# Performance work log

Hardware: AMD Instinct MI355X
Metric: run time of the kernel (lower is better)

## Reference

```python
import jax, jax.numpy as jnp
import numpy as np
import math

B, T, D, H = 4, 1024, 1024, 16
DK = D // H
TAU_THRESH = 0.3


def setup_inputs() -> dict:
    key = jax.random.key(0)
    ks = jax.random.split(key, 13)
    s = 1.0 / math.sqrt(D)
    return {
        "x": jax.random.normal(ks[0], (B, T, D), dtype=jnp.float32),
        "Wq": jax.random.normal(ks[1], (D, D), dtype=jnp.float32) * s,
        "bq": jax.random.normal(ks[2], (D,), dtype=jnp.float32) * s,
        "Wk": jax.random.normal(ks[3], (D, D), dtype=jnp.float32) * s,
        "bk": jax.random.normal(ks[4], (D,), dtype=jnp.float32) * s,
        "Wv": jax.random.normal(ks[5], (D, D), dtype=jnp.float32) * s,
        "bv": jax.random.normal(ks[6], (D,), dtype=jnp.float32) * s,
        "Wo": jax.random.normal(ks[7], (D, D), dtype=jnp.float32) * s,
        "bo": jax.random.normal(ks[8], (D,), dtype=jnp.float32) * s,
        "Wg1": jax.random.normal(ks[9], (1, D), dtype=jnp.float32) * s,
        "bg1": jax.random.normal(ks[10], (1,), dtype=jnp.float32) * s,
        "Wg2": jax.random.normal(ks[11], (1, D), dtype=jnp.float32) * s,
        "bg2": jax.random.normal(ks[12], (1,), dtype=jnp.float32) * s,
    }


def reference(x, Wq, bq, Wk, bk, Wv, bv, Wo, bo, Wg1, bg1, Wg2, bg2):
    b, t, d = x.shape
    # projections (torch Linear: y = x @ W.T + b)
    Q = (x @ Wq.T + bq).reshape(b, t, H, DK).transpose(0, 2, 1, 3)  # [B,H,T,dk]
    K = (x @ Wk.T + bk).reshape(b, t, H, DK).transpose(0, 2, 1, 3)
    V = (x @ Wv.T + bv).reshape(b, t, H, DK).transpose(0, 2, 1, 3)
    scores = jnp.einsum("bhqd,bhkd->bhqk", Q, K) / math.sqrt(DK)  # [B,H,T,T]
    # confidence gates from first-token query context [B, H*dk] = [B, D]
    context = Q[:, :, 0, :].reshape(b, d)
    q1 = jax.nn.sigmoid(context @ Wg1.T + bg1)  # [B,1]
    q2 = jax.nn.sigmoid(context @ Wg2.T + bg2)  # [B,1]
    c = jnp.clip(q1 * q2, 1e-8, 1.0)            # [B,1]
    tau = jnp.where(c < TAU_THRESH, 1.0 / c, jnp.ones_like(c)).reshape(b, 1, 1, 1)
    p = jax.nn.softmax(scores / tau, axis=-1)
    cb = c.reshape(b, 1, 1, 1)
    p_gated = cb * p + (1.0 - cb) * (1.0 / t)
    u = jnp.mean(1.0 - c, axis=-1, keepdims=True)  # [B,1]
    attn_out = jnp.einsum("bhqk,bhkd->bhqd", p_gated, V)
    attn_out = attn_out.transpose(0, 2, 1, 3).reshape(b, t, d)
    output = attn_out @ Wo.T + bo
    return output, u
```

## Files before the change

kernel.cpp:

```cpp
#include <hip/hip_runtime.h>
#include <stdint.h>

typedef short bf16x8 __attribute__((ext_vector_type(8)));
typedef float f32x4 __attribute__((ext_vector_type(4)));

#define MFMA_BF16(a, b, c) __builtin_amdgcn_mfma_f32_16x16x32_bf16((a), (b), (c), 0, 0, 0)

__device__ __forceinline__ short f2bf(float x) {
  union { float f; uint32_t u; } v; v.f = x;
  uint32_t r = (v.u + 0x7FFFu + ((v.u >> 16) & 1u)) >> 16;
  return (short)r;
}
__device__ __forceinline__ uint32_t rnd_bf_hi(float x) {
  union { float f; uint32_t u; } v; v.f = x;
  return v.u + 0x7FFFu + ((v.u >> 16) & 1u);
}
__device__ __forceinline__ uint32_t pack2bf(float a, float b) {
  return __builtin_amdgcn_perm(rnd_bf_hi(b), rnd_bf_hi(a), 0x07060302);
}
__device__ __forceinline__ float bfbits2f(uint32_t b16) {
  union { uint32_t u; float f; } v; v.u = b16 << 16; return v.f;
}
__device__ __forceinline__ float fexp2(float x) {
#if __has_builtin(__builtin_amdgcn_exp2f)
  return __builtin_amdgcn_exp2f(x);
#else
  return __expf(x * 0.6931471805599453f);
#endif
}
__device__ __forceinline__ void async16(const void* g, void* l) {
  __builtin_amdgcn_global_load_lds(
      (const __attribute__((address_space(1))) uint32_t*)g,
      (__attribute__((address_space(3))) uint32_t*)l, 16, 0, 0);
}

__global__ __launch_bounds__(256) void prep_k(
    const float* __restrict__ x, const float* __restrict__ Wq,
    const float* __restrict__ Wk, const float* __restrict__ Wv,
    const float* __restrict__ Wo, const float* __restrict__ bq,
    short* __restrict__ xb, short* __restrict__ Wqb, short* __restrict__ Wkb,
    short* __restrict__ Wvb, short* __restrict__ Wob, float* __restrict__ ctx) {
  __shared__ float xs[1024];
  const int bid = blockIdx.x;
  const int tid = threadIdx.x;
  if (bid < 8192) {
    const float* src; short* dst; int idx;
    if (bid < 4096) {
      src = x; dst = xb; idx = (bid << 8) + tid;
    } else {
      const int r = bid - 4096;
      const int z = r >> 10;
      src = (z == 0) ? Wq : (z == 1) ? Wk : (z == 2) ? Wv : Wo;
      dst = (z == 0) ? Wqb : (z == 1) ? Wkb : (z == 2) ? Wvb : Wob;
      idx = ((r & 1023) << 8) + tid;
    }
    float4 v = ((const float4*)src)[idx];
    short4 o;
    o.x = f2bf(v.x); o.y = f2bf(v.y); o.z = f2bf(v.z); o.w = f2bf(v.w);
    ((short4*)dst)[idx] = o;
  } else {
    const int r = bid - 8192;
    const int b = r >> 4;
    const int n0 = (r & 15) << 6;
    for (int i = tid; i < 1024; i += 256) xs[i] = x[b * 1048576 + i];
    __syncthreads();
    const int w = tid >> 6, lane = tid & 63;
    const float4* xv4 = (const float4*)xs;
    for (int rr = 0; rr < 16; ++rr) {
      const int n = n0 + (w << 4) + rr;
      const float4* wrow = (const float4*)(Wq + n * 1024);
      float p = 0.f;
#pragma unroll
      for (int c2 = 0; c2 < 4; ++c2) {
        float4 wv = wrow[lane + (c2 << 6)];
        float4 xv = xv4[lane + (c2 << 6)];
        p += xv.x * wv.x + xv.y * wv.y + xv.z * wv.z + xv.w * wv.w;
      }
#pragma unroll
      for (int off = 32; off; off >>= 1) p += __shfl_xor(p, off);
      if (lane == 0) ctx[b * 1024 + n] = p + bq[n];
    }
  }
}

__global__ __launch_bounds__(256) void gates_fin(const float* __restrict__ ctx,
                                                 const float* __restrict__ Wg1,
                                                 const float* __restrict__ bg1,
                                                 const float* __restrict__ Wg2,
                                                 const float* __restrict__ bg2,
                                                 float* __restrict__ gates,
                                                 float* __restrict__ u_out) {
  __shared__ float red[16];
  const int tid = threadIdx.x, w = tid >> 6, lane = tid & 63;
  for (int b = 0; b < 4; ++b) {
    float4 cv = ((const float4*)(ctx + b * 1024))[tid];
    float4 w1 = ((const float4*)Wg1)[tid];
    float4 w2 = ((const float4*)Wg2)[tid];
    float p1 = cv.x * w1.x + cv.y * w1.y + cv.z * w1.z + cv.w * w1.w;
    float p2 = cv.x * w2.x + cv.y * w2.y + cv.z * w2.z + cv.w * w2.w;
#pragma unroll
    for (int off = 32; off; off >>= 1) { p1 += __shfl_xor(p1, off); p2 += __shfl_xor(p2, off); }
    if (lane == 0) { red[w] = p1; red[8 + w] = p2; }
    __syncthreads();
    if (tid == 0) {
      float g1 = red[0] + red[1] + red[2] + red[3] + bg1[0];
      float g2 = red[8] + red[9] + red[10] + red[11] + bg2[0];
      float q1 = 1.f / (1.f + expf(-g1));
      float q2 = 1.f / (1.f + expf(-g2));
      float c = fminf(fmaxf(q1 * q2, 1e-8f), 1.0f);
      gates[b * 2 + 0] = c;
      gates[b * 2 + 1] = (c < 0.3f ? c : 1.0f) * 0.125f;
      u_out[b] = 1.0f - c;
    }
    __syncthreads();
  }
}

__global__ __launch_bounds__(256) void gemm_qkv(
    const short* __restrict__ xb,
    const short* __restrict__ Wqb, const short* __restrict__ Wkb, const short* __restrict__ Wvb,
    const float* __restrict__ bq, const float* __restrict__ bk, const float* __restrict__ bv,
    const float* __restrict__ gat,
    short* __restrict__ Qh, short* __restrict__ Kh, short* __restrict__ Vt) {
  const int z = blockIdx.z;
  const short* W = (z == 0) ? Wqb : (z == 1) ? Wkb : Wvb;
  const float* bias = (z == 0) ? bq : (z == 1) ? bk : bv;

  const int m0 = blockIdx.x << 7;
  const int n0 = blockIdx.y << 7;
  const int tid = threadIdx.x;
  const int w = tid >> 6, lane = tid & 63;
  const int m15 = lane & 15, quad = lane >> 4;
  const int wr = w >> 1, wc = w & 1;

  const float qsc = (z == 0) ? gat[(m0 >> 10) * 2 + 1] * 1.4426950408889634f : 1.0f;

  __shared__ short As[4096];
  __shared__ short Bs[4096];

  f32x4 acc[4][4];
#pragma unroll
  for (int i = 0; i < 4; ++i)
#pragma unroll
    for (int j = 0; j < 4; ++j) { f32x4 zz = {0.f, 0.f, 0.f, 0.f}; acc[i][j] = zz; }

  const int s0 = tid, s1 = tid + 256;
  const int row0 = s0 >> 2, lcb0 = (s0 & 3) ^ ((row0 >> 1) & 3);
  const int row1 = s1 >> 2, lcb1 = (s1 & 3) ^ ((row1 >> 1) & 3);
  const short* ga0 = xb + (m0 + row0) * 1024 + (lcb0 << 3);
  const short* ga1 = xb + (m0 + row1) * 1024 + (lcb1 << 3);
  const short* gb0 = W + (n0 + row0) * 1024 + (lcb0 << 3);
  const short* gb1 = W + (n0 + row1) * 1024 + (lcb1 << 3);
  short* la0 = &As[s0 << 3];
  short* la1 = &As[s1 << 3];
  short* lb0 = &Bs[s0 << 3];
  short* lb1 = &Bs[s1 << 3];

  for (int kt = 0; kt < 32; ++kt) {
    async16(ga0, la0); async16(ga1, la1);
    async16(gb0, lb0); async16(gb1, lb1);
    ga0 += 32; ga1 += 32; gb0 += 32; gb1 += 32;
    __syncthreads();
    bf16x8 a[4], b[4];
#pragma unroll
    for (int i = 0; i < 4; ++i) {
      const int ra = (wr << 6) + (i << 4) + m15;
      a[i] = *(const bf16x8*)(&As[ra * 32 + ((quad ^ ((ra >> 1) & 3)) << 3)]);
    }
#pragma unroll
    for (int j = 0; j < 4; ++j) {
      const int rb = (wc << 6) + (j << 4) + m15;
      b[j] = *(const bf16x8*)(&Bs[rb * 32 + ((quad ^ ((rb >> 1) & 3)) << 3)]);
    }
#pragma unroll
    for (int i = 0; i < 4; ++i)
#pragma unroll
      for (int j = 0; j < 4; ++j)
        acc[i][j] = MFMA_BF16(a[i], b[j], acc[i][j]);
    __syncthreads();
  }

  if (z == 2) {
    const int batch = m0 >> 10;
#pragma unroll
    for (int j = 0; j < 4; ++j) {
      const int n = n0 + (wc << 6) + (j << 4) + m15;
      const float bb_ = bias[n];
      const int h = n >> 6, dk = n & 63;
      short* vrow = Vt + ((((batch << 4) + h) << 6) + dk) * 1024;
#pragma unroll
      for (int i = 0; i < 4; ++i) {
        const int t = (m0 & 1023) + (wr << 6) + (i << 4) + (quad << 2);
        uint2 pk;
        pk.x = pack2bf(acc[i][j][0] + bb_, acc[i][j][1] + bb_);
        pk.y = pack2bf(acc[i][j][2] + bb_, acc[i][j][3] + bb_);
        *(uint2*)(vrow + t) = pk;
      }
    }
  } else {
#pragma unroll
    for (int j = 0; j < 4; ++j) {
      const int n = n0 + (wc << 6) + (j << 4) + m15;
      const float bb_ = bias[n];
      const int h = n >> 6, dk = n & 63;
#pragma unroll
      for (int i = 0; i < 4; ++i) {
        const int mb = m0 + (wr << 6) + (i << 4) + (quad << 2);
#pragma unroll
        for (int r = 0; r < 4; ++r) {
          const int m = mb + r;
          const int batch = m >> 10, t = m & 1023;
          const short o = f2bf((acc[i][j][r] + bb_) * qsc);
          if (z == 1) Kh[((batch * 16 + h) * 1024 + t) * 64 + dk] = o;
          else        Qh[((batch * 16 + h) * 1024 + t) * 64 + dk] = o;
        }
      }
    }
  }
}

__global__ __launch_bounds__(256) void gemm_out(const short* __restrict__ Ab,
                                                const short* __restrict__ Wo,
                                                const float* __restrict__ bo,
                                                float* __restrict__ Cout) {
  const int m0 = blockIdx.x << 6;
  const int n0 = blockIdx.y << 7;
  const int tid = threadIdx.x;
  const int w = tid >> 6, lane = tid & 63;
  const int m15 = lane & 15, quad = lane >> 4;
  const int wr = w >> 1, wc = w & 1;

  __shared__ short As[2048];
  __shared__ short Bs[4096];

  f32x4 acc[2][4];
#pragma unroll
  for (int i = 0; i < 2; ++i)
#pragma unroll
    for (int j = 0; j < 4; ++j) { f32x4 zz = {0.f, 0.f, 0.f, 0.f}; acc[i][j] = zz; }

  const int s0 = tid, s1 = tid + 256;
  const int arow = s0 >> 2, alcb = (s0 & 3) ^ ((arow >> 1) & 3);
  const int brow0 = s0 >> 2, blcb0 = alcb;
  const int brow1 = s1 >> 2, blcb1 = (s1 & 3) ^ ((brow1 >> 1) & 3);
  const short* gA  = Ab + (m0 + arow) * 1024 + (alcb << 3);
  const short* gB0 = Wo + (n0 + brow0) * 1024 + (blcb0 << 3);
  const short* gB1 = Wo + (n0 + brow1) * 1024 + (blcb1 << 3);
  short* lA  = &As[s0 << 3];
  short* lB0 = &Bs[s0 << 3];
  short* lB1 = &Bs[s1 << 3];

  for (int kt = 0; kt < 32; ++kt) {
    async16(gA, lA);
    async16(gB0, lB0); async16(gB1, lB1);
    gA += 32; gB0 += 32; gB1 += 32;
    __syncthreads();
    bf16x8 a[2], b[4];
#pragma unroll
    for (int i = 0; i < 2; ++i) {
      const int ra = (wr << 5) + (i << 4) + m15;
      a[i] = *(const bf16x8*)(&As[ra * 32 + ((quad ^ ((ra >> 1) & 3)) << 3)]);
    }
#pragma unroll
    for (int j = 0; j < 4; ++j) {
      const int rb = (wc << 6) + (j << 4) + m15;
      b[j] = *(const bf16x8*)(&Bs[rb * 32 + ((quad ^ ((rb >> 1) & 3)) << 3)]);
    }
#pragma unroll
    for (int i = 0; i < 2; ++i)
#pragma unroll
      for (int j = 0; j < 4; ++j)
        acc[i][j] = MFMA_BF16(a[i], b[j], acc[i][j]);
    __syncthreads();
  }

#pragma unroll
  for (int j = 0; j < 4; ++j) {
    const int n = n0 + (wc << 6) + (j << 4) + m15;
    const float bb_ = bo[n];
#pragma unroll
    for (int i = 0; i < 2; ++i) {
      const int mb = m0 + (wr << 5) + (i << 4) + (quad << 2);
#pragma unroll
      for (int r = 0; r < 4; ++r)
        Cout[(mb + r) * 1024 + n] = acc[i][j][r] + bb_;
    }
  }
}

__global__ __launch_bounds__(256) void meanv_k(const short* __restrict__ Vt,
                                               float* __restrict__ meanV) {
  const int bh = blockIdx.x;
  const int tid = threadIdx.x;
  const int d = tid >> 2, part = tid & 3;
  const short* row = Vt + bh * 65536 + d * 1024 + part * 256;
  float s = 0.f;
#pragma unroll 4
  for (int i = 0; i < 64; ++i) {
    uint2 v = *(const uint2*)(row + i * 4);
    s += bfbits2f(v.x & 0xffffu) + bfbits2f(v.x >> 16) +
         bfbits2f(v.y & 0xffffu) + bfbits2f(v.y >> 16);
  }
  s += __shfl_xor(s, 1);
  s += __shfl_xor(s, 2);
  if (part == 0) meanV[bh * 64 + d] = s * (1.0f / 1024.0f);
}

__global__ __launch_bounds__(256, 4) void attn_k(const short* __restrict__ Qh,
                                                 const short* __restrict__ Kh,
                                                 const short* __restrict__ Vt,
                                                 const float* __restrict__ gates,
                                                 const float* __restrict__ meanV,
                                                 short* __restrict__ attnb) {
  const int bh = blockIdx.x;
  const int b = bh >> 4, h = bh & 15;
  const int q0 = blockIdx.y << 6;
  const int tid = threadIdx.x;
  const int w = tid >> 6, lane = tid & 63;
  const int m15 = lane & 15, quad = lane >> 4;

  __shared__ short Ks[2][4096];
  __shared__ short Vs[2][4096];

  const short* ksrc = Kh + bh * 65536;
  const short* vsrc = Vt + bh * 65536;

  const short* qsrc = Qh + ((bh << 10) + q0 + (w << 4) + m15) * 64;
  const bf16x8 qb0 = *(const bf16x8*)(qsrc + (quad << 3));
  const bf16x8 qb1 = *(const bf16x8*)(qsrc + 32 + (quad << 3));

  const int off0 = tid, off1 = tid + 256;
  const int r0 = off0 >> 3, cb0 = (off0 & 7) ^ (r0 & 7);
  const int r1 = off1 >> 3, cb1 = (off1 & 7) ^ (r1 & 7);

#define STAGE(kv, bufi)                                                        \
  do {                                                                         \
    async16(ksrc + (((kv) << 6) + r0) * 64 + (cb0 << 3), &Ks[bufi][off0 << 3]);\
    async16(ksrc + (((kv) << 6) + r1) * 64 + (cb1 << 3), &Ks[bufi][off1 << 3]);\
    async16(vsrc + r0 * 1024 + ((kv) << 6) + (cb0 << 3), &Vs[bufi][off0 << 3]);\
    async16(vsrc + r1 * 1024 + ((kv) << 6) + (cb1 << 3), &Vs[bufi][off1 << 3]);\
  } while (0)

  STAGE(0, 0);

  float lsum = 0.f;
  f32x4 o_acc[4];
#pragma unroll
  for (int jd = 0; jd < 4; ++jd) { f32x4 zz = {0.f, 0.f, 0.f, 0.f}; o_acc[jd] = zz; }

  const int srcA = ((quad & 1) << 5) + m15;
  const int srcB = srcA + 16;
  const bool selhi = (quad & 2) != 0;

  for (int kv = 0; kv < 16; ++kv) {
    __syncthreads();
    if (kv < 15) STAGE(kv + 1, (kv + 1) & 1);
    const short* Kb = &Ks[kv & 1][0];
    const short* Vb = &Vs[kv & 1][0];

    f32x4 sacc[4];
#pragma unroll
    for (int s = 0; s < 4; ++s) {
      const int row = (s << 4) + m15;
      const int sw = row & 7;
      bf16x8 a0 = *(const bf16x8*)(Kb + (row << 6) + ((quad ^ sw) << 3));
      bf16x8 a1 = *(const bf16x8*)(Kb + (row << 6) + (((quad + 4) ^ sw) << 3));
      f32x4 zz = {0.f, 0.f, 0.f, 0.f};
      zz = MFMA_BF16(a0, qb0, zz);
      zz = MFMA_BF16(a1, qb1, zz);
      sacc[s] = zz;
    }

    uint32_t pk[4][2];
#pragma unroll
    for (int s = 0; s < 4; ++s) {
      float p0 = fexp2(sacc[s][0]);
      float p1 = fexp2(sacc[s][1]);
      float p2 = fexp2(sacc[s][2]);
      float p3 = fexp2(sacc[s][3]);
      lsum += (p0 + p1) + (p2 + p3);
      pk[s][0] = pack2bf(p0, p1);
      pk[s][1] = pack2bf(p2, p3);
    }

    bf16x8 pf[2];
#pragma unroll
    for (int H = 0; H < 2; ++H) {
      uint32_t f[4];
#pragma unroll
      for (int rp = 0; rp < 2; ++rp) {
        uint32_t alo = (uint32_t)__shfl((int)pk[2 * H][rp], srcA);
        uint32_t ahi = (uint32_t)__shfl((int)pk[2 * H + 1][rp], srcA);
        uint32_t blo = (uint32_t)__shfl((int)pk[2 * H][rp], srcB);
        uint32_t bhi = (uint32_t)__shfl((int)pk[2 * H + 1][rp], srcB);
        f[rp]     = selhi ? ahi : alo;
        f[2 + rp] = selhi ? bhi : blo;
      }
      pf[H] = *(bf16x8*)f;
    }

#pragma unroll
    for (int jd = 0; jd < 4; ++jd) {
      const int row = (jd << 4) + m15;
      const int sw = row & 7;
      bf16x8 v0 = *(const bf16x8*)(Vb + (row << 6) + ((quad ^ sw) << 3));
      bf16x8 v1 = *(const bf16x8*)(Vb + (row << 6) + (((quad + 4) ^ sw) << 3));
      o_acc[jd] = MFMA_BF16(v0, pf[0], o_acc[jd]);
      o_acc[jd] = MFMA_BF16(v1, pf[1], o_acc[jd]);
    }
  }
#undef STAGE

  float l = lsum;
  l += __shfl_xor(l, 16);
  l += __shfl_xor(l, 32);

  const float cg = gates[b * 2 + 0];
  const float s0 = cg / l;
  const float omc = 1.0f - cg;
  const int qrow = q0 + (w << 4) + m15;
  short* orow = attnb + ((b << 10) + qrow) * 1024 + (h << 6);
#pragma unroll
  for (int jd = 0; jd < 4; ++jd) {
    float4 mv = *(const float4*)(meanV + (bh << 6) + (jd << 4) + (quad << 2));
    float v0_ = s0 * o_acc[jd][0] + omc * mv.x;
    float v1_ = s0 * o_acc[jd][1] + omc * mv.y;
    float v2_ = s0 * o_acc[jd][2] + omc * mv.z;
    float v3_ = s0 * o_acc[jd][3] + omc * mv.w;
    uint2 st;
    st.x = pack2bf(v0_, v1_);
    st.y = pack2bf(v2_, v3_);
    *(uint2*)(orow + (jd << 4) + (quad << 2)) = st;
  }
}

extern "C" void kernel_launch(void* const* d_in, const int* in_sizes, int n_in,
                              void* d_out, int out_size, void* d_ws, size_t ws_size,
                              hipStream_t stream) {
  const float* x   = (const float*)d_in[0];
  const float* Wq  = (const float*)d_in[1];
  const float* bq  = (const float*)d_in[2];
  const float* Wk  = (const float*)d_in[3];
  const float* bk  = (const float*)d_in[4];
  const float* Wv  = (const float*)d_in[5];
  const float* bv  = (const float*)d_in[6];
  const float* Wo  = (const float*)d_in[7];
  const float* bo  = (const float*)d_in[8];
  const float* Wg1 = (const float*)d_in[9];
  const float* bg1 = (const float*)d_in[10];
  const float* Wg2 = (const float*)d_in[11];
  const float* bg2 = (const float*)d_in[12];
  float* out = (float*)d_out;

  char* ws = (char*)d_ws;
  short* xb   = (short*)(ws + 0);
  short* Wqb  = (short*)(ws + 8388608);
  short* Wkb  = (short*)(ws + 10485760);
  short* Wvb  = (short*)(ws + 12582912);
  short* Wob  = (short*)(ws + 14680064);
  short* Qh   = (short*)(ws + 16777216);
  short* Kh   = (short*)(ws + 25165824);
  short* Vt   = (short*)(ws + 33554432);
  short* attb = (short*)(ws + 41943040);
  float* ctx  = (float*)(ws + 50331648);
  float* gat  = (float*)(ws + 50348032);
  float* mV   = (float*)(ws + 50348064);

  prep_k<<<8256, 256, 0, stream>>>(x, Wq, Wk, Wv, Wo, bq,
                                   xb, Wqb, Wkb, Wvb, Wob, ctx);
  gates_fin<<<1, 256, 0, stream>>>(ctx, Wg1, bg1, Wg2, bg2, gat, out + 4194304);

  gemm_qkv<<<dim3(32, 8, 3), 256, 0, stream>>>(xb, Wqb, Wkb, Wvb, bq, bk, bv, gat, Qh, Kh, Vt);
  meanv_k<<<64, 256, 0, stream>>>(Vt, mV);
  attn_k<<<dim3(64, 16), 256, 0, stream>>>(Qh, Kh, Vt, gat, mV, attb);
  gemm_out<<<dim3(64, 8), 256, 0, stream>>>(attb, Wob, bo, out);
}
```

Before: 218.6 us.

## Fuse V-mean into QKV GEMM epilogue and shrink QKV tile to 64 rows

Removes the separate meanv kernel by accumulating per-column V sums with atomics in the QKV GEMM epilogue, zeroed by a memset. The QKV GEMM M-tile drops from 128 to 64, doubling the grid to 1536 blocks. The softmax temperature scale moves from the Q store into the attention exp path (one extra multiply per score element). This removes a kernel launch and a read of V, but adds atomics and lowers per-block data reuse in the GEMM.

Result: no change. 217.6 us (-0.5%).

```diff
diff --git a/kernel.cpp b/kernel.cpp
--- a/kernel.cpp
+++ b/kernel.cpp
@@ -109,7 +109,7 @@
       float q2 = 1.f / (1.f + expf(-g2));
       float c = fminf(fmaxf(q1 * q2, 1e-8f), 1.0f);
       gates[b * 2 + 0] = c;
-      gates[b * 2 + 1] = (c < 0.3f ? c : 1.0f) * 0.125f;
+      gates[b * 2 + 1] = (c < 0.3f ? c : 1.0f) * 0.125f * 1.4426950408889634f;
       u_out[b] = 1.0f - c;
     }
     __syncthreads();
@@ -120,51 +120,47 @@
     const short* __restrict__ xb,
     const short* __restrict__ Wqb, const short* __restrict__ Wkb, const short* __restrict__ Wvb,
     const float* __restrict__ bq, const float* __restrict__ bk, const float* __restrict__ bv,
-    const float* __restrict__ gat,
-    short* __restrict__ Qh, short* __restrict__ Kh, short* __restrict__ Vt) {
+    short* __restrict__ Qh, short* __restrict__ Kh, short* __restrict__ Vt,
+    float* __restrict__ mV) {
   const int z = blockIdx.z;
   const short* W = (z == 0) ? Wqb : (z == 1) ? Wkb : Wvb;
   const float* bias = (z == 0) ? bq : (z == 1) ? bk : bv;
 
-  const int m0 = blockIdx.x << 7;
+  const int m0 = blockIdx.x << 6;
   const int n0 = blockIdx.y << 7;
   const int tid = threadIdx.x;
   const int w = tid >> 6, lane = tid & 63;
   const int m15 = lane & 15, quad = lane >> 4;
   const int wr = w >> 1, wc = w & 1;
 
-  const float qsc = (z == 0) ? gat[(m0 >> 10) * 2 + 1] * 1.4426950408889634f : 1.0f;
-
-  __shared__ short As[4096];
+  __shared__ short As[2048];
   __shared__ short Bs[4096];
 
-  f32x4 acc[4][4];
-#pragma unroll
-  for (int i = 0; i < 4; ++i)
+  f32x4 acc[2][4];
+#pragma unroll
+  for (int i = 0; i < 2; ++i)
 #pragma unroll
     for (int j = 0; j < 4; ++j) { f32x4 zz = {0.f, 0.f, 0.f, 0.f}; acc[i][j] = zz; }
 
   const int s0 = tid, s1 = tid + 256;
-  const int row0 = s0 >> 2, lcb0 = (s0 & 3) ^ ((row0 >> 1) & 3);
-  const int row1 = s1 >> 2, lcb1 = (s1 & 3) ^ ((row1 >> 1) & 3);
-  const short* ga0 = xb + (m0 + row0) * 1024 + (lcb0 << 3);
-  const short* ga1 = xb + (m0 + row1) * 1024 + (lcb1 << 3);
-  const short* gb0 = W + (n0 + row0) * 1024 + (lcb0 << 3);
-  const short* gb1 = W + (n0 + row1) * 1024 + (lcb1 << 3);
-  short* la0 = &As[s0 << 3];
-  short* la1 = &As[s1 << 3];
-  short* lb0 = &Bs[s0 << 3];
-  short* lb1 = &Bs[s1 << 3];
+  const int arow = s0 >> 2, alcb = (s0 & 3) ^ ((arow >> 1) & 3);
+  const int brow1 = s1 >> 2, blcb1 = (s1 & 3) ^ ((brow1 >> 1) & 3);
+  const short* gA  = xb + (m0 + arow) * 1024 + (alcb << 3);
+  const short* gB0 = W + (n0 + arow) * 1024 + (alcb << 3);
+  const short* gB1 = W + (n0 + brow1) * 1024 + (blcb1 << 3);
+  short* lA  = &As[s0 << 3];
+  short* lB0 = &Bs[s0 << 3];
+  short* lB1 = &Bs[s1 << 3];
 
   for (int kt = 0; kt < 32; ++kt) {
-    async16(ga0, la0); async16(ga1, la1);
-    async16(gb0, lb0); async16(gb1, lb1);
-    ga0 += 32; ga1 += 32; gb0 += 32; gb1 += 32;
-    __syncthreads();
-    bf16x8 a[4], b[4];
-#pragma unroll
-    for (int i = 0; i < 4; ++i) {
-      const int ra = (wr << 6) + (i << 4) + m15;
+    async16(gA, lA);
+    async16(gB0, lB0); async16(gB1, lB1);
+    gA += 32; gB0 += 32; gB1 += 32;
+    __syncthreads();
+    bf16x8 a[2], b[4];
+#pragma unroll
+    for (int i = 0; i < 2; ++i) {
+      const int ra = (wr << 5) + (i << 4) + m15;
       a[i] = *(const bf16x8*)(&As[ra * 32 + ((quad ^ ((ra >> 1) & 3)) << 3)]);
     }
 #pragma unroll
@@ -173,7 +169,7 @@
       b[j] = *(const bf16x8*)(&Bs[rb * 32 + ((quad ^ ((rb >> 1) & 3)) << 3)]);
     }
 #pragma unroll
-    for (int i = 0; i < 4; ++i)
+    for (int i = 0; i < 2; ++i)
 #pragma unroll
       for (int j = 0; j < 4; ++j)
         acc[i][j] = MFMA_BF16(a[i], b[j], acc[i][j]);
@@ -188,14 +184,19 @@
       const float bb_ = bias[n];
       const int h = n >> 6, dk = n & 63;
       short* vrow = Vt + ((((batch << 4) + h) << 6) + dk) * 1024;
-#pragma unroll
-      for (int i = 0; i < 4; ++i) {
-        const int t = (m0 & 1023) + (wr << 6) + (i << 4) + (quad << 2);
+      float msum = 8.0f * bb_;
+#pragma unroll
+      for (int i = 0; i < 2; ++i) {
+        const int t = (m0 & 1023) + (wr << 5) + (i << 4) + (quad << 2);
         uint2 pk;
         pk.x = pack2bf(acc[i][j][0] + bb_, acc[i][j][1] + bb_);
         pk.y = pack2bf(acc[i][j][2] + bb_, acc[i][j][3] + bb_);
         *(uint2*)(vrow + t) = pk;
+        msum += (acc[i][j][0] + acc[i][j][1]) + (acc[i][j][2] + acc[i][j][3]);
       }
+      msum += __shfl_xor(msum, 16);
+      msum += __shfl_xor(msum, 32);
+      if (quad == 0) atomicAdd(&mV[(((batch << 4) + h) << 6) + dk], msum);
     }
   } else {
 #pragma unroll
@@ -204,13 +205,13 @@
       const float bb_ = bias[n];
       const int h = n >> 6, dk = n & 63;
 #pragma unroll
-      for (int i = 0; i < 4; ++i) {
-        const int mb = m0 + (wr << 6) + (i << 4) + (quad << 2);
+      for (int i = 0; i < 2; ++i) {
+        const int mb = m0 + (wr << 5) + (i << 4) + (quad << 2);
 #pragma unroll
         for (int r = 0; r < 4; ++r) {
           const int m = mb + r;
           const int batch = m >> 10, t = m & 1023;
-          const short o = f2bf((acc[i][j][r] + bb_) * qsc);
+          const short o = f2bf(acc[i][j][r] + bb_);
           if (z == 1) Kh[((batch * 16 + h) * 1024 + t) * 64 + dk] = o;
           else        Qh[((batch * 16 + h) * 1024 + t) * 64 + dk] = o;
         }
@@ -241,10 +242,9 @@
 
   const int s0 = tid, s1 = tid + 256;
   const int arow = s0 >> 2, alcb = (s0 & 3) ^ ((arow >> 1) & 3);
-  const int brow0 = s0 >> 2, blcb0 = alcb;
   const int brow1 = s1 >> 2, blcb1 = (s1 & 3) ^ ((brow1 >> 1) & 3);
   const short* gA  = Ab + (m0 + arow) * 1024 + (alcb << 3);
-  const short* gB0 = Wo + (n0 + brow0) * 1024 + (blcb0 << 3);
+  const short* gB0 = Wo + (n0 + arow) * 1024 + (alcb << 3);
   const short* gB1 = Wo + (n0 + brow1) * 1024 + (blcb1 << 3);
   short* lA  = &As[s0 << 3];
   short* lB0 = &Bs[s0 << 3];
@@ -288,29 +288,11 @@
   }
 }
 
-__global__ __launch_bounds__(256) void meanv_k(const short* __restrict__ Vt,
-                                               float* __restrict__ meanV) {
-  const int bh = blockIdx.x;
-  const int tid = threadIdx.x;
-  const int d = tid >> 2, part = tid & 3;
-  const short* row = Vt + bh * 65536 + d * 1024 + part * 256;
-  float s = 0.f;
-#pragma unroll 4
-  for (int i = 0; i < 64; ++i) {
-    uint2 v = *(const uint2*)(row + i * 4);
-    s += bfbits2f(v.x & 0xffffu) + bfbits2f(v.x >> 16) +
-         bfbits2f(v.y & 0xffffu) + bfbits2f(v.y >> 16);
-  }
-  s += __shfl_xor(s, 1);
-  s += __shfl_xor(s, 2);
-  if (part == 0) meanV[bh * 64 + d] = s * (1.0f / 1024.0f);
-}
-
 __global__ __launch_bounds__(256, 4) void attn_k(const short* __restrict__ Qh,
                                                  const short* __restrict__ Kh,
                                                  const short* __restrict__ Vt,
                                                  const float* __restrict__ gates,
-                                                 const float* __restrict__ meanV,
+                                                 const float* __restrict__ mV,
                                                  short* __restrict__ attnb) {
   const int bh = blockIdx.x;
   const int b = bh >> 4, h = bh & 15;
@@ -324,6 +306,8 @@
 
   const short* ksrc = Kh + bh * 65536;
   const short* vsrc = Vt + bh * 65536;
+
+  const float sl = gates[b * 2 + 1];
 
   const short* qsrc = Qh + ((bh << 10) + q0 + (w << 4) + m15) * 64;
   const bf16x8 qb0 = *(const bf16x8*)(qsrc + (quad << 3));
@@ -374,10 +358,10 @@
     uint32_t pk[4][2];
 #pragma unroll
     for (int s = 0; s < 4; ++s) {
-      float p0 = fexp2(sacc[s][0]);
-      float p1 = fexp2(sacc[s][1]);
-      float p2 = fexp2(sacc[s][2]);
-      float p3 = fexp2(sacc[s][3]);
+      float p0 = fexp2(sacc[s][0] * sl);
+      float p1 = fexp2(sacc[s][1] * sl);
+      float p2 = fexp2(sacc[s][2] * sl);
+      float p3 = fexp2(sacc[s][3] * sl);
       lsum += (p0 + p1) + (p2 + p3);
       pk[s][0] = pack2bf(p0, p1);
       pk[s][1] = pack2bf(p2, p3);
@@ -417,16 +401,16 @@
 
   const float cg = gates[b * 2 + 0];
   const float s0 = cg / l;
-  const float omc = 1.0f - cg;
+  const float coef = (1.0f - cg) * (1.0f / 1024.0f);
   const int qrow = q0 + (w << 4) + m15;
   short* orow = attnb + ((b << 10) + qrow) * 1024 + (h << 6);
 #pragma unroll
   for (int jd = 0; jd < 4; ++jd) {
-    float4 mv = *(const float4*)(meanV + (bh << 6) + (jd << 4) + (quad << 2));
-    float v0_ = s0 * o_acc[jd][0] + omc * mv.x;
-    float v1_ = s0 * o_acc[jd][1] + omc * mv.y;
-    float v2_ = s0 * o_acc[jd][2] + omc * mv.z;
-    float v3_ = s0 * o_acc[jd][3] + omc * mv.w;
+    float4 mv = *(const float4*)(mV + (bh << 6) + (jd << 4) + (quad << 2));
+    float v0_ = s0 * o_acc[jd][0] + coef * mv.x;
+    float v1_ = s0 * o_acc[jd][1] + coef * mv.y;
+    float v2_ = s0 * o_acc[jd][2] + coef * mv.z;
+    float v3_ = s0 * o_acc[jd][3] + coef * mv.w;
     uint2 st;
     st.x = pack2bf(v0_, v1_);
     st.y = pack2bf(v2_, v3_);
@@ -466,12 +450,14 @@
   float* gat  = (float*)(ws + 50348032);
   float* mV   = (float*)(ws + 50348064);
 
+  hipMemsetAsync(mV, 0, 64 * 64 * sizeof(float), stream);
+
   prep_k<<<8256, 256, 0, stream>>>(x, Wq, Wk, Wv, Wo, bq,
                                    xb, Wqb, Wkb, Wvb, Wob, ctx);
   gates_fin<<<1, 256, 0, stream>>>(ctx, Wg1, bg1, Wg2, bg2, gat, out + 4194304);
 
-  gemm_qkv<<<dim3(32, 8, 3), 256, 0, stream>>>(xb, Wqb, Wkb, Wvb, bq, bk, bv, gat, Qh, Kh, Vt);
-  meanv_k<<<64, 256, 0, stream>>>(Vt, mV);
+  gemm_qkv<<<dim3(64, 8, 3), 256, 0, stream>>>(xb, Wqb, Wkb, Wvb, bq, bk, bv,
+                                               Qh, Kh, Vt, mV);
   attn_k<<<dim3(64, 16), 256, 0, stream>>>(Qh, Kh, Vt, gat, mV, attb);
   gemm_out<<<dim3(64, 8), 256, 0, stream>>>(attb, Wob, bo, out);
 }
```
